# Optimization experiments

Hardware: AMD Instinct MI355X
Metric: run time of the kernel (lower is better)

The kernel has to match this reference:

```python
import jax, jax.numpy as jnp
import numpy as np

EMBED = 1024
HEADS = 16
HEAD_DIM = EMBED // HEADS


def setup_inputs() -> dict:
    key = jax.random.key(0)
    ks = jax.random.split(key, 8)
    B, S, D = 4, 2048, EMBED
    s = 1.0 / np.sqrt(D)
    return {
        "values": jax.random.normal(ks[0], (B, S, D), jnp.float32),
        "keys": jax.random.normal(ks[1], (B, S, D), jnp.float32),
        "query": jax.random.normal(ks[2], (B, S, D), jnp.float32),
        "Wv": jax.random.normal(ks[3], (D, D), jnp.float32) * s,
        "Wk": jax.random.normal(ks[4], (D, D), jnp.float32) * s,
        "Wq": jax.random.normal(ks[5], (D, D), jnp.float32) * s,
        "Wo": jax.random.normal(ks[6], (D, D), jnp.float32) * s,
        "bo": jax.random.normal(ks[7], (D,), jnp.float32) * 0.01,
    }


def reference(values, keys, query, Wv, Wk, Wq, Wo, bo):
    N, Lq, D = query.shape
    Lk = keys.shape[1]
    Lv = values.shape[1]
    # torch Linear: y = x @ W.T
    v = (values @ Wv.T).reshape(N, Lv, HEADS, HEAD_DIM)
    k = (keys @ Wk.T).reshape(N, Lk, HEADS, HEAD_DIM)
    q = (query @ Wq.T).reshape(N, Lq, HEADS, HEAD_DIM)
    energy = jnp.einsum('nqhd,nkhd->nhqk', q, k)
    # NOTE: module scales by 1/sqrt(embed_size), not 1/sqrt(head_dim)
    attn = jax.nn.softmax(energy / jnp.sqrt(jnp.float32(D)), axis=3)
    out = jnp.einsum('nhql,nlhd->nqhd', attn, v).reshape(N, Lq, D)
    return out @ Wo.T + bo
```

## Files before the change

kernel.cpp:

```cpp
#include <hip/hip_runtime.h>
#include <cstdint>
#include <cstddef>


typedef unsigned short ushortT;
typedef __bf16 bf16x8 __attribute__((ext_vector_type(8)));
typedef _Float16 f16x4 __attribute__((ext_vector_type(4)));
typedef float f32x4 __attribute__((ext_vector_type(4)));
typedef unsigned int u32x2 __attribute__((ext_vector_type(2)));
typedef unsigned short us4 __attribute__((ext_vector_type(4)));
typedef unsigned short us8 __attribute__((ext_vector_type(8)));

#define S_LEN 2048
#define NB 4
#define NH 16
#define HD 64
#define DMODEL 1024
#define MTOT 8192
#define WSZ 1048576

#define AS1 __attribute__((address_space(1)))
#define AS3 __attribute__((address_space(3)))

__device__ __forceinline__ ushortT f2b(float f) {
  unsigned x = __builtin_bit_cast(unsigned, f);
  x += 0x7fffu + ((x >> 16) & 1u);
  return (ushortT)(x >> 16);
}

__device__ __forceinline__ unsigned rne_pack(unsigned lo, unsigned hi) {
  lo += 0x7fffu + ((lo >> 16) & 1u);
  hi += 0x7fffu + ((hi >> 16) & 1u);
  return __builtin_amdgcn_perm(hi, lo, 0x07060302u);
}

__device__ __forceinline__ f32x4 mfma_bf16(bf16x8 a, bf16x8 b, f32x4 c) {
  return __builtin_amdgcn_mfma_f32_16x16x32_bf16(a, b, c, 0, 0, 0);
}
__device__ __forceinline__ f32x4 mfma16_f16(f16x4 a, f16x4 b, f32x4 c) {
  return __builtin_amdgcn_mfma_f32_16x16x16f16(a, b, c, 0, 0, 0);
}

__device__ __forceinline__ void gl2lds16(const ushortT* g, ushortT* l) {
  __builtin_amdgcn_global_load_lds((const AS1 void*)g, (AS3 void*)l, 16, 0, 0);
}

__global__ __launch_bounds__(256) void convert_w_kernel(
    const float* __restrict__ wq, const float* __restrict__ wk,
    const float* __restrict__ wv, const float* __restrict__ wo,
    ushortT* __restrict__ dst) {
  const float* s;
  switch (blockIdx.y) {
    case 0: s = wq; break;
    case 1: s = wk; break;
    case 2: s = wv; break;
    default: s = wo; break;
  }
  ushortT* d = dst + (size_t)blockIdx.y * WSZ;
  const size_t i = ((size_t)blockIdx.x * 256 + threadIdx.x) * 8;
  uint4 w0 = *(const uint4*)(s + i);
  uint4 w1 = *(const uint4*)(s + i + 4);
  uint4 pk;
  pk.x = rne_pack(w0.x, w0.y);
  pk.y = rne_pack(w0.z, w0.w);
  pk.z = rne_pack(w1.x, w1.y);
  pk.w = rne_pack(w1.z, w1.w);
  *(uint4*)(d + i) = pk;
}

__global__ __launch_bounds__(256) void convert_x_kernel(
    const float* __restrict__ vals, const float* __restrict__ keys,
    const float* __restrict__ qry, ushortT* __restrict__ dst) {
  const float* s;
  switch (blockIdx.y) {
    case 0: s = vals; break;
    case 1: s = keys; break;
    default: s = qry; break;
  }
  ushortT* d = dst + (size_t)blockIdx.y * ((size_t)MTOT * DMODEL);
  const size_t i = ((size_t)blockIdx.x * 256 + threadIdx.x) * 8;
  uint4 w0 = *(const uint4*)(s + i);
  uint4 w1 = *(const uint4*)(s + i + 4);
  uint4 pk;
  pk.x = rne_pack(w0.x, w0.y);
  pk.y = rne_pack(w0.z, w0.w);
  pk.z = rne_pack(w1.x, w1.y);
  pk.w = rne_pack(w1.z, w1.w);
  *(uint4*)(d + i) = pk;
}

template <int VT_MODE, bool A_F32, bool OUT_F32, bool HAS_BIAS, int ASTR,
          int NW>
__device__ __forceinline__ void gemm_bt_tile(const void* __restrict__ A,
                                             const ushortT* __restrict__ W,
                                             const float* __restrict__ bias,
                                             void* __restrict__ C, float oscale,
                                             ushortT* __restrict__ As,
                                             ushortT* __restrict__ Bs) {
  constexpr int K = 1024, N = 1024;
  constexpr int NI = (NW == 4) ? 4 : 2;
  constexpr int CPT = 8 / NW;
  static_assert(!A_F32 || NW == 4, "f32 A staging implemented for 4 waves");
  static_assert(A_F32 || ASTR == 32, "gl2lds A staging requires linear rows");
  const int tid = threadIdx.x;
  const int wave = tid >> 6, lane = tid & 63, quad = lane >> 4, l16 = lane & 15;
  const int wm = wave & 1, wn = wave >> 1;
  const int by = blockIdx.x, bx = blockIdx.y;

  const size_t Aoff = (size_t)by * 128 * K;
  const ushortT* Wb = W + (size_t)bx * 128 * K;

  const f32x4 fz = {0.f, 0.f, 0.f, 0.f};
  f32x4 acc[4][NI];
#pragma unroll
  for (int mi = 0; mi < 4; mi++)
#pragma unroll
    for (int ni = 0; ni < NI; ni++) acc[mi][ni] = fz;

  for (int kt = 0; kt < K; kt += 32) {
    __syncthreads();
#pragma unroll
    for (int i = 0; i < CPT; ++i) {
      const int cb = (wave * CPT + i) * 64;
      const int c = cb + lane;
      const int m = c >> 2, ko = c & 3;
      gl2lds16(Wb + (size_t)m * K + kt + ko * 8, Bs + (size_t)cb * 8);
    }
    if (A_F32) {
#pragma unroll
      for (int j = 0; j < 2; ++j) {
        const int c = tid + j * 256;
        const int m = c >> 2, ko = c & 3;
        const float* ap = (const float*)A + Aoff + (size_t)m * K + kt + ko * 8;
        uint4 w0 = *(const uint4*)ap;
        uint4 w1 = *(const uint4*)(ap + 4);
        uint4 pk;
        pk.x = rne_pack(w0.x, w0.y);
        pk.y = rne_pack(w0.z, w0.w);
        pk.z = rne_pack(w1.x, w1.y);
        pk.w = rne_pack(w1.z, w1.w);
        *(uint4*)(As + (size_t)m * ASTR + ko * 8) = pk;
      }
    } else {
#pragma unroll
      for (int i = 0; i < CPT; ++i) {
        const int cb = (wave * CPT + i) * 64;
        const int c = cb + lane;
        const int m = c >> 2, ko = c & 3;
        gl2lds16((const ushortT*)A + Aoff + (size_t)m * K + kt + ko * 8,
                 As + (size_t)cb * 8);
      }
    }
    __syncthreads();

    bf16x8 af[4], bfr[NI];
#pragma unroll
    for (int mi = 0; mi < 4; mi++)
      af[mi] =
          *(const bf16x8*)(As + (wm * 64 + mi * 16 + l16) * ASTR + quad * 8);
#pragma unroll
    for (int ni = 0; ni < NI; ni++)
      bfr[ni] = *(const bf16x8*)(Bs + (wn * (NI * 16) + ni * 16 + l16) * 32 +
                                 quad * 8);
#pragma unroll
    for (int mi = 0; mi < 4; mi++)
#pragma unroll
      for (int ni = 0; ni < NI; ni++)
        acc[mi][ni] = mfma_bf16(af[mi], bfr[ni], acc[mi][ni]);
  }

#pragma unroll
  for (int mi = 0; mi < 4; mi++) {
    const int row0 = by * 128 + wm * 64 + mi * 16 + quad * 4;
#pragma unroll
    for (int ni = 0; ni < NI; ni++) {
      const int col = bx * 128 + wn * (NI * 16) + ni * 16 + l16;
      const float bv = HAS_BIAS ? bias[col] : 0.f;
      if (VT_MODE == 0) {
#pragma unroll
        for (int i = 0; i < 4; i++) {
          const size_t idx = (size_t)(row0 + i) * N + col;
          const float val = acc[mi][ni][i] * oscale + bv;
          if (OUT_F32)
            ((float*)C)[idx] = val;
          else
            ((ushortT*)C)[idx] = f2b(val);
        }
      } else {
        const int h = col >> 6, dd = col & 63;
        const int bb = row0 >> 11, s0 = row0 & (S_LEN - 1);
        u32x2 pk;
        pk[0] = __builtin_bit_cast(
            unsigned, __builtin_amdgcn_cvt_pkrtz(acc[mi][ni][0], acc[mi][ni][1]));
        pk[1] = __builtin_bit_cast(
            unsigned, __builtin_amdgcn_cvt_pkrtz(acc[mi][ni][2], acc[mi][ni][3]));
        *(u32x2*)((ushortT*)C + ((size_t)((bb * NH + h) * HD + dd) << 11) + s0) =
            pk;
      }
    }
  }
}

__global__ __launch_bounds__(256) void qkv_proj_bf16_kernel(
    const ushortT* __restrict__ xb, const ushortT* __restrict__ wcat,
    ushortT* __restrict__ qb, ushortT* __restrict__ kb,
    ushortT* __restrict__ vtb) {
  __shared__ alignas(16) ushortT As[128 * 32];
  __shared__ alignas(16) ushortT Bs[128 * 32];
  const size_t E = (size_t)MTOT * DMODEL;
  const int z = blockIdx.z;
  const float QSC = 1.44269504088896f / 32.0f;
  if (z == 0)
    gemm_bt_tile<0, false, false, false, 32, 4>(xb + 2 * E, wcat, nullptr, qb,
                                                QSC, As, Bs);
  else if (z == 1)
    gemm_bt_tile<0, false, false, false, 32, 4>(xb + E, wcat + WSZ, nullptr,
                                                kb, 1.0f, As, Bs);
  else
    gemm_bt_tile<1, false, false, false, 32, 4>(xb, wcat + 2 * WSZ, nullptr,
                                                vtb, 1.0f, As, Bs);
}

__global__ __launch_bounds__(256) void qkv_proj_kernel(
    const float* __restrict__ vals, const float* __restrict__ keys,
    const float* __restrict__ qry, const ushortT* __restrict__ wcat,
    ushortT* __restrict__ qb, ushortT* __restrict__ kb,
    ushortT* __restrict__ vtb) {
  __shared__ alignas(16) ushortT As[128 * 40];
  __shared__ alignas(16) ushortT Bs[128 * 32];
  const int z = blockIdx.z;
  const float QSC = 1.44269504088896f / 32.0f;
  if (z == 0)
    gemm_bt_tile<0, true, false, false, 40, 4>(qry, wcat, nullptr, qb, QSC, As,
                                               Bs);
  else if (z == 1)
    gemm_bt_tile<0, true, false, false, 40, 4>(keys, wcat + WSZ, nullptr, kb,
                                               1.0f, As, Bs);
  else
    gemm_bt_tile<1, true, false, false, 40, 4>(vals, wcat + 2 * WSZ, nullptr,
                                               vtb, 1.0f, As, Bs);
}

__global__ __launch_bounds__(512) void out_proj_kernel(
    const ushortT* __restrict__ ain, const ushortT* __restrict__ wo,
    const float* __restrict__ bo, float* __restrict__ out) {
  __shared__ alignas(16) ushortT As[128 * 32];
  __shared__ alignas(16) ushortT Bs[128 * 32];
  gemm_bt_tile<0, false, true, true, 32, 8>(ain, wo, bo, out, 1.0f, As, Bs);
}

__global__ __launch_bounds__(256) void attn_kernel(
    const ushortT* __restrict__ qb, const ushortT* __restrict__ kb,
    const ushortT* __restrict__ vtb, ushortT* __restrict__ ab) {
  __shared__ alignas(16) ushortT Ks[128 * 72];
  __shared__ alignas(16) ushortT Vts[64 * 136];

  const int tid = threadIdx.x;
  const int wave = tid >> 6, lane = tid & 63, quad = lane >> 4, l16 = lane & 15;
  const int bh = blockIdx.x, qt = blockIdx.y, b = bh >> 4, h = bh & 15;

  bf16x8 qf[2][2];
#pragma unroll
  for (int mi = 0; mi < 2; mi++)
#pragma unroll
    for (int kq = 0; kq < 2; kq++) {
      const int qrow = qt * 128 + wave * 32 + mi * 16 + l16;
      qf[mi][kq] = *(const bf16x8*)(qb + (size_t)(b * S_LEN + qrow) * DMODEL +
                                    h * HD + kq * 32 + quad * 8);
    }

  const f32x4 fz = {0.f, 0.f, 0.f, 0.f};
  f32x4 osum[4][2];
#pragma unroll
  for (int ni = 0; ni < 4; ni++)
#pragma unroll
    for (int mi = 0; mi < 2; mi++) osum[ni][mi] = fz;
  float lsum[2] = {0.f, 0.f};

  us8 kreg[4], vreg[4];
  auto issue_loads = [&](int t) {
#pragma unroll
    for (int p = 0; p < 4; p++) {
      const int r = (tid >> 3) + p * 32, c = (tid & 7) * 8;
      kreg[p] = *(const us8*)(kb + (size_t)(b * S_LEN + t * 128 + r) * DMODEL +
                              h * HD + c);
    }
#pragma unroll
    for (int p = 0; p < 4; p++) {
      const int r = (tid >> 4) + p * 16, c = (tid & 15) * 8;
      vreg[p] = *(const us8*)(vtb + (size_t)((b * NH + h) * HD + r) * S_LEN +
                              t * 128 + c);
    }
  };
  issue_loads(0);

  for (int t = 0; t < 16; ++t) {
    __syncthreads();
#pragma unroll
    for (int p = 0; p < 4; p++) {
      const int r = (tid >> 3) + p * 32, c = (tid & 7) * 8;
      *(us8*)(Ks + r * 72 + c) = kreg[p];
    }
#pragma unroll
    for (int p = 0; p < 4; p++) {
      const int r = (tid >> 4) + p * 16, c = (tid & 15) * 8;
      *(us8*)(Vts + r * 136 + c) = vreg[p];
    }
    if (t < 15) issue_loads(t + 1);
    __syncthreads();

#pragma unroll
    for (int h2 = 0; h2 < 2; ++h2) {
      f32x4 sacc[4][2];
#pragma unroll
      for (int mt = 0; mt < 4; mt++)
#pragma unroll
        for (int mi = 0; mi < 2; mi++) sacc[mt][mi] = fz;
      __builtin_amdgcn_s_setprio(1);
#pragma unroll
      for (int kq = 0; kq < 2; kq++)
#pragma unroll
        for (int mt = 0; mt < 4; mt++) {
          bf16x8 kf = *(const bf16x8*)(Ks + ((h2 * 4 + mt) * 16 + l16) * 72 +
                                       kq * 32 + quad * 8);
#pragma unroll
          for (int mi = 0; mi < 2; mi++)
            sacc[mt][mi] = mfma_bf16(kf, qf[mi][kq], sacc[mt][mi]);
        }
      __builtin_amdgcn_s_setprio(0);

      u32x2 pf[4][2];
#pragma unroll
      for (int mt = 0; mt < 4; mt++)
#pragma unroll
        for (int mi = 0; mi < 2; mi++) {
          const float e0 = __builtin_amdgcn_exp2f(sacc[mt][mi][0]);
          const float e1 = __builtin_amdgcn_exp2f(sacc[mt][mi][1]);
          const float e2 = __builtin_amdgcn_exp2f(sacc[mt][mi][2]);
          const float e3 = __builtin_amdgcn_exp2f(sacc[mt][mi][3]);
          lsum[mi] += (e0 + e1) + (e2 + e3);
          pf[mt][mi][0] =
              __builtin_bit_cast(unsigned, __builtin_amdgcn_cvt_pkrtz(e0, e1));
          pf[mt][mi][1] =
              __builtin_bit_cast(unsigned, __builtin_amdgcn_cvt_pkrtz(e2, e3));
        }

      __builtin_amdgcn_s_setprio(1);
#pragma unroll
      for (int s = 0; s < 4; ++s)
#pragma unroll
        for (int ni = 0; ni < 4; ni++) {
          f16x4 vf = *(const f16x4*)(Vts + (ni * 16 + l16) * 136 +
                                     (h2 * 4 + s) * 16 + quad * 4);
#pragma unroll
          for (int mi = 0; mi < 2; mi++)
            osum[ni][mi] =
                mfma16_f16(vf, __builtin_bit_cast(f16x4, pf[s][mi]), osum[ni][mi]);
        }
      __builtin_amdgcn_s_setprio(0);
    }
  }

#pragma unroll
  for (int mi = 0; mi < 2; mi++) {
    float s = lsum[mi];
    s += __shfl_xor(s, 16, 64);
    s += __shfl_xor(s, 32, 64);
    lsum[mi] = 1.0f / s;
  }

#pragma unroll
  for (int mi = 0; mi < 2; mi++) {
    const int qrow = qt * 128 + wave * 32 + mi * 16 + l16;
#pragma unroll
    for (int ni = 0; ni < 4; ni++) {
      us4 pk;
#pragma unroll
      for (int i = 0; i < 4; i++) pk[i] = f2b(osum[ni][mi][i] * lsum[mi]);
      *(us4*)(ab + (size_t)(b * S_LEN + qrow) * DMODEL + h * HD + ni * 16 +
              quad * 4) = pk;
    }
  }
}

extern "C" void kernel_launch(void* const* d_in, const int* in_sizes, int n_in,
                              void* d_out, int out_size, void* d_ws,
                              size_t ws_size, hipStream_t stream) {
  const float* vals = (const float*)d_in[0];
  const float* keys = (const float*)d_in[1];
  const float* qry = (const float*)d_in[2];
  const float* Wv = (const float*)d_in[3];
  const float* Wk = (const float*)d_in[4];
  const float* Wq = (const float*)d_in[5];
  const float* Wo = (const float*)d_in[6];
  const float* bo = (const float*)d_in[7];
  float* out = (float*)d_out;

  ushortT* ws = (ushortT*)d_ws;
  const size_t E = (size_t)MTOT * DMODEL;
  ushortT* qbuf = ws;
  ushortT* kbuf = ws + E;
  ushortT* vtb = ws + 2 * E;
  ushortT* wcat = ws + 3 * E;
  ushortT* xb = ws + 3 * E + 4 * (size_t)WSZ;
  ushortT* abuf = qbuf;

  const size_t need = (6 * E + 4 * (size_t)WSZ) * sizeof(ushortT);

  dim3 blk(256, 1, 1);
  convert_w_kernel<<<dim3(512, 4), blk, 0, stream>>>(Wq, Wk, Wv, Wo, wcat);
  if (ws_size >= need) {
    convert_x_kernel<<<dim3(4096, 3), blk, 0, stream>>>(vals, keys, qry, xb);
    qkv_proj_bf16_kernel<<<dim3(64, 8, 3), blk, 0, stream>>>(xb, wcat, qbuf,
                                                             kbuf, vtb);
  } else {
    qkv_proj_kernel<<<dim3(64, 8, 3), blk, 0, stream>>>(vals, keys, qry, wcat,
                                                        qbuf, kbuf, vtb);
  }
  attn_kernel<<<dim3(64, 16), blk, 0, stream>>>(qbuf, kbuf, vtb, abuf);
  out_proj_kernel<<<dim3(64, 8), dim3(512, 1, 1), 0, stream>>>(
      abuf, wcat + 3 * WSZ, bo, out);
}
```

Measured before the change: 344.3 us.

## Load attention K/V tiles directly into LDS with XOR-swizzled layout

Replaces the register-staged K and V^T tile loads (global to registers, then registers to padded LDS) with direct global-to-LDS 16-byte loads into unpadded tiles. An XOR swizzle on the 8-element chunk index replaces the padding as the guard against bank conflicts. This removes the register round trip and frees VGPRs. It also drops the software prefetch of the next tile, so global load latency is no longer overlapped with compute and is exposed before each barrier.

```diff
diff --git a/kernel.cpp b/kernel.cpp
--- a/kernel.cpp
+++ b/kernel.cpp
@@ -252,8 +252,8 @@
 __global__ __launch_bounds__(256) void attn_kernel(
     const ushortT* __restrict__ qb, const ushortT* __restrict__ kb,
     const ushortT* __restrict__ vtb, ushortT* __restrict__ ab) {
-  __shared__ alignas(16) ushortT Ks[128 * 72];
-  __shared__ alignas(16) ushortT Vts[64 * 136];
+  __shared__ alignas(16) ushortT Ks[128 * 64];
+  __shared__ alignas(16) ushortT Vts[64 * 128];
 
   const int tid = threadIdx.x;
   const int wave = tid >> 6, lane = tid & 63, quad = lane >> 4, l16 = lane & 15;
@@ -277,36 +277,25 @@
     for (int mi = 0; mi < 2; mi++) osum[ni][mi] = fz;
   float lsum[2] = {0.f, 0.f};
 
-  us8 kreg[4], vreg[4];
-  auto issue_loads = [&](int t) {
-#pragma unroll
-    for (int p = 0; p < 4; p++) {
-      const int r = (tid >> 3) + p * 32, c = (tid & 7) * 8;
-      kreg[p] = *(const us8*)(kb + (size_t)(b * S_LEN + t * 128 + r) * DMODEL +
-                              h * HD + c);
-    }
-#pragma unroll
-    for (int p = 0; p < 4; p++) {
-      const int r = (tid >> 4) + p * 16, c = (tid & 15) * 8;
-      vreg[p] = *(const us8*)(vtb + (size_t)((b * NH + h) * HD + r) * S_LEN +
-                              t * 128 + c);
-    }
-  };
-  issue_loads(0);
+  const ushortT* kbb = kb + (size_t)b * S_LEN * DMODEL + h * HD;
+  const ushortT* vbb = vtb + (size_t)(b * NH + h) * HD * S_LEN;
 
   for (int t = 0; t < 16; ++t) {
     __syncthreads();
 #pragma unroll
-    for (int p = 0; p < 4; p++) {
-      const int r = (tid >> 3) + p * 32, c = (tid & 7) * 8;
-      *(us8*)(Ks + r * 72 + c) = kreg[p];
-    }
-#pragma unroll
-    for (int p = 0; p < 4; p++) {
-      const int r = (tid >> 4) + p * 16, c = (tid & 15) * 8;
-      *(us8*)(Vts + r * 136 + c) = vreg[p];
-    }
-    if (t < 15) issue_loads(t + 1);
+    for (int i = 0; i < 4; ++i) {
+      const int cb = (wave * 4 + i) * 64;
+      const int c = cb + lane;
+      const int r = c >> 3, lch = (c & 7) ^ (r & 7);
+      gl2lds16(kbb + (size_t)(t * 128 + r) * DMODEL + lch * 8, Ks + cb * 8);
+    }
+#pragma unroll
+    for (int i = 0; i < 4; ++i) {
+      const int cb = (wave * 4 + i) * 64;
+      const int c = cb + lane;
+      const int r = c >> 4, lch = (c & 15) ^ (r & 15);
+      gl2lds16(vbb + (size_t)r * S_LEN + t * 128 + lch * 8, Vts + cb * 8);
+    }
     __syncthreads();
 
 #pragma unroll
@@ -321,8 +310,9 @@
       for (int kq = 0; kq < 2; kq++)
 #pragma unroll
         for (int mt = 0; mt < 4; mt++) {
-          bf16x8 kf = *(const bf16x8*)(Ks + ((h2 * 4 + mt) * 16 + l16) * 72 +
-                                       kq * 32 + quad * 8);
+          const int krow = (h2 * 4 + mt) * 16 + l16;
+          const int kch = (kq * 4 + quad) ^ (krow & 7);
+          bf16x8 kf = *(const bf16x8*)(Ks + krow * 64 + kch * 8);
 #pragma unroll
           for (int mi = 0; mi < 2; mi++)
             sacc[mt][mi] = mfma_bf16(kf, qf[mi][kq], sacc[mt][mi]);
@@ -350,8 +340,10 @@
       for (int s = 0; s < 4; ++s)
 #pragma unroll
         for (int ni = 0; ni < 4; ni++) {
-          f16x4 vf = *(const f16x4*)(Vts + (ni * 16 + l16) * 136 +
-                                     (h2 * 4 + s) * 16 + quad * 4);
+          const int vrow = ni * 16 + l16;
+          const int vch = ((h2 * 4 + s) * 2 + (quad >> 1)) ^ (vrow & 15);
+          f16x4 vf = *(const f16x4*)(Vts + vrow * 128 + vch * 8 +
+                                     (quad & 1) * 4);
 #pragma unroll
           for (int mi = 0; mi < 2; mi++)
             osum[ni][mi] =
```

Measured after the change: 339.9 us. About the same (-1.3%).
